# Performance work log

Hardware: AMD Instinct MI355X
Metric: run time of the kernel (lower is better)

The kernel has to match this reference:

```python
import jax, jax.numpy as jnp
import numpy as np

B, S, D, H = 2, 2048, 1024, 16
HD = D // H  # head_dim = 64
ROPE_BASE = 10000.0
INIT_STD = 0.02


def setup_inputs() -> dict:
    key = jax.random.key(0)
    k1, k2, k3 = jax.random.split(key, 3)
    x = jax.random.normal(k1, (B, S, D), dtype=jnp.float32)
    w_qkv = jax.random.normal(k2, (3 * D, D), dtype=jnp.float32) * INIT_STD
    w_out = jax.random.normal(k3, (D, D), dtype=jnp.float32) * (1.0 / np.sqrt(D))
    b_out = jnp.zeros((D,), dtype=jnp.float32)
    return {"x": x, "w_qkv": w_qkv, "w_out": w_out, "b_out": b_out}


def _rope_cos_sin(s_len, head_dim, dtype):
    theta = 1.0 / ROPE_BASE ** (jnp.arange(0, head_dim, 2, dtype=jnp.float32) / head_dim)
    freqs = jnp.outer(jnp.arange(s_len, dtype=jnp.float32), theta)  # [s, d/2]
    freqs = jnp.concatenate([freqs, freqs], axis=-1)  # [s, d]
    return jnp.cos(freqs).astype(dtype), jnp.sin(freqs).astype(dtype)


def _apply_rope(qk, cos, sin):
    # qk: [b, h, s, d]; rotate-half: (-x2, x1)
    d2 = qk.shape[-1] // 2
    x1, x2 = qk[..., :d2], qk[..., d2:]
    rot = jnp.concatenate([-x2, x1], axis=-1)
    return qk * cos + rot * sin


def reference(x, w_qkv, w_out, b_out):
    b, s, d = x.shape
    qkv = jnp.einsum('bsd,ed->bse', x, w_qkv)  # [b, s, 3D]
    qkv = qkv.reshape(b, s, 3 * H, HD).transpose(0, 2, 1, 3)  # [b, 3h, s, d]
    qk, v = qkv[:, :2 * H], qkv[:, 2 * H:]
    cos, sin = _rope_cos_sin(s, HD, x.dtype)
    qk = _apply_rope(qk, cos, sin)
    q, k = qk[:, :H], qk[:, H:]
    scale = 1.0 / np.sqrt(HD)
    scores = jnp.einsum('bhqd,bhkd->bhqk', q, k) * scale  # [b, h, s, s]
    causal = jnp.tril(jnp.ones((s, s), dtype=bool))
    scores = jnp.where(causal, scores, jnp.finfo(scores.dtype).min)
    attn = jax.nn.softmax(scores, axis=-1)
    o = jnp.einsum('bhqk,bhkd->bhqd', attn, v)  # [b, h, s, d]
    o = o.transpose(0, 2, 1, 3).reshape(b, s, d)
    return jnp.einsum('bsd,ed->bse', o, w_out) + b_out
```

## Files before the change

kernel.cpp:

```cpp
#include <hip/hip_runtime.h>
#include <hip/hip_fp16.h>
#include <math.h>

#define B_  2
#define S_  2048
#define D_  1024
#define H_  16
#define HD_ 64

typedef _Float16  f16;
typedef __attribute__((ext_vector_type(8))) _Float16 f16x8;
typedef __attribute__((ext_vector_type(4))) _Float16 f16x4;
typedef __attribute__((ext_vector_type(4))) float    f32x4;

#define LOG2E 1.4426950408889634f
#define L2_10000_DIV32 0.41524101186092029f

__device__ __forceinline__ float fin(float v) { return (v == v) ? v : 0.0f; }

__device__ __forceinline__ f16x8 cvt8(const float* p) {
  float4 a = *(const float4*)p;
  float4 b = *(const float4*)(p + 4);
  f16x8 h;
  h[0] = (f16)a.x; h[1] = (f16)a.y; h[2] = (f16)a.z; h[3] = (f16)a.w;
  h[4] = (f16)b.x; h[5] = (f16)b.y; h[6] = (f16)b.z; h[7] = (f16)b.w;
  return h;
}

__device__ __forceinline__ int swz64(int r, int c) {
  return r * 64 + ((((c >> 3) ^ (r & 7)) << 3) | (c & 7));
}

#define GLD16(g, l)                                                        \
  __builtin_amdgcn_global_load_lds(                                        \
      (const __attribute__((address_space(1))) void*)(g),                  \
      (__attribute__((address_space(3))) void*)(l), 16, 0, 0)

__global__ void __launch_bounds__(256)
k_cvt3(const float* __restrict__ wq, const float* __restrict__ wo,
       const float* __restrict__ x,
       f16* __restrict__ wqh, f16* __restrict__ woh, f16* __restrict__ xh,
       float2* __restrict__ tab, int doX)
{
  const int NWQ = 3 * D_ * D_ / 4, NWO = D_ * D_ / 4, NX = B_ * S_ * D_ / 4;
  const int n = NWQ + NWO + (doX ? NX : 0);
  for (int i = blockIdx.x * 256 + threadIdx.x; i < n; i += gridDim.x * 256) {
    const float* src; f16* dst; int j;
    if (i < NWQ)            { src = wq; dst = wqh; j = i; }
    else if (i < NWQ + NWO) { src = wo; dst = woh; j = i - NWQ; }
    else                    { src = x;  dst = xh;  j = i - NWQ - NWO; }
    float4 v = ((const float4*)src)[j];
    f16x4 h = {(f16)v.x, (f16)v.y, (f16)v.z, (f16)v.w};
    ((f16x4*)dst)[j] = h;
  }
  for (int i = blockIdx.x * 256 + threadIdx.x; i < S_ * 32; i += gridDim.x * 256) {
    const int p = i >> 5, j = i & 31;
    const float th = exp2f(-(float)j * L2_10000_DIV32);
    float s, c;
    sincosf((float)p * th, &s, &c);
    tab[i] = make_float2(c, s);
  }
}

template <bool XF16>
__global__ void __launch_bounds__(256)
k_qkv4(const float* __restrict__ xf, const f16* __restrict__ xh,
       const f16* __restrict__ wqh, const float2* __restrict__ tab,
       f16* __restrict__ Qb, f16* __restrict__ Kb, f16* __restrict__ Vt)
{
  __shared__ __align__(16) f16 As[2][128 * 64];
  __shared__ __align__(16) f16 Bs[2][128 * 64];
  const int t = threadIdx.x;
  const int w = t >> 6;
  const int lane = t & 63;
  const int ll = lane & 15;
  const int quad = lane >> 4;
  const int wm = w >> 1, wn = w & 1;
  const int row0 = blockIdx.y * 128;
  const int col0 = blockIdx.x * 128;

  const f32x4 fz = {0.f, 0.f, 0.f, 0.f};
  f32x4 acc[4][4];
#pragma unroll
  for (int i = 0; i < 4; ++i)
#pragma unroll
    for (int j = 0; j < 4; ++j) acc[i][j] = fz;

  const int rO = lane >> 3;
  const int gc = (lane & 7) ^ rO;
  const f16* pA = xh  + (size_t)(row0 + w * 8 + rO) * D_ + gc * 8;
  const f16* pB = wqh + (size_t)(col0 + w * 8 + rO) * D_ + gc * 8;
  const int ldst = (w * 8) * 64;

  const int raA0 = swz64(ll, quad * 8);
  const int raA1 = swz64(ll, 32 + quad * 8);

  const int ldr = t >> 3;
  const int ldk = (t & 7) * 8;
  const float* gaf = xf + (size_t)(row0 + ldr) * D_ + ldk;

  if (XF16) {
#pragma unroll
    for (int i = 0; i < 4; ++i) {
      GLD16(pA + (size_t)(i * 32) * D_, &As[0][i * 32 * 64 + ldst]);
      GLD16(pB + (size_t)(i * 32) * D_, &Bs[0][i * 32 * 64 + ldst]);
    }
    __syncthreads();
    pA += 64; pB += 64;

    for (int kt = 0; kt < 16; ++kt) {
      const int cur = kt & 1, nxt = cur ^ 1;
      if (kt < 15) {
#pragma unroll
        for (int i = 0; i < 4; ++i) {
          GLD16(pA + (size_t)(i * 32) * D_, &As[nxt][i * 32 * 64 + ldst]);
          GLD16(pB + (size_t)(i * 32) * D_, &Bs[nxt][i * 32 * 64 + ldst]);
        }
        pA += 64; pB += 64;
      }
      const f16* Ac = &As[cur][0];
      const f16* Bc = &Bs[cur][0];
#pragma unroll
      for (int kk = 0; kk < 2; ++kk) {
        const int ro = kk ? raA1 : raA0;
        f16x8 a[4], b[4];
#pragma unroll
        for (int mt = 0; mt < 4; ++mt)
          a[mt] = *(const f16x8*)&Ac[(wm * 64 + mt * 16) * 64 + ro];
#pragma unroll
        for (int nt = 0; nt < 4; ++nt)
          b[nt] = *(const f16x8*)&Bc[(wn * 64 + nt * 16) * 64 + ro];
#pragma unroll
        for (int mt = 0; mt < 4; ++mt)
#pragma unroll
          for (int nt = 0; nt < 4; ++nt)
            acc[mt][nt] = __builtin_amdgcn_mfma_f32_16x16x32_f16(
                a[mt], b[nt], acc[mt][nt], 0, 0, 0);
      }
      __syncthreads();
    }
  } else {
    for (int kt = 0; kt < D_; kt += 64) {
      f16x8 ra[4];
#pragma unroll
      for (int i = 0; i < 4; ++i)
        ra[i] = cvt8(gaf + (size_t)i * 32 * D_ + kt);
      __syncthreads();
#pragma unroll
      for (int i = 0; i < 4; ++i) {
        *(f16x8*)&As[0][swz64(i * 32 + ldr, ldk)] = ra[i];
        GLD16(pB + (size_t)(i * 32) * D_ + kt, &Bs[0][i * 32 * 64 + ldst]);
      }
      __syncthreads();
#pragma unroll
      for (int kk = 0; kk < 2; ++kk) {
        const int ro = kk ? raA1 : raA0;
        f16x8 a[4], b[4];
#pragma unroll
        for (int mt = 0; mt < 4; ++mt)
          a[mt] = *(const f16x8*)&As[0][(wm * 64 + mt * 16) * 64 + ro];
#pragma unroll
        for (int nt = 0; nt < 4; ++nt)
          b[nt] = *(const f16x8*)&Bs[0][(wn * 64 + nt * 16) * 64 + ro];
#pragma unroll
        for (int mt = 0; mt < 4; ++mt)
#pragma unroll
          for (int nt = 0; nt < 4; ++nt)
            acc[mt][nt] = __builtin_amdgcn_mfma_f32_16x16x32_f16(
                a[mt], b[nt], acc[mt][nt], 0, 0, 0);
      }
      __syncthreads();
    }
  }

  const int h3 = (col0 >> 6) + wn;
  if (h3 < 32) {
    f16* dst = (h3 < 16) ? Qb : Kb;
    const int h = (h3 < 16) ? h3 : h3 - 16;
#pragma unroll
    for (int mt = 0; mt < 4; ++mt) {
#pragma unroll
      for (int r = 0; r < 4; ++r) {
        const int row = row0 + wm * 64 + mt * 16 + quad * 4 + r;
        const int b = row >> 11;
        const int p = row & (S_ - 1);
        f16* base = dst + ((size_t)(b * H_ + h) * S_ + p) * HD_;
        const float2 cs0 = tab[p * 32 + ll];
        const float2 cs1 = tab[p * 32 + 16 + ll];
        {
          float x1 = acc[mt][0][r], x2 = acc[mt][2][r];
          base[ll]      = (f16)fin(x1 * cs0.x - x2 * cs0.y);
          base[ll + 32] = (f16)fin(x2 * cs0.x + x1 * cs0.y);
        }
        {
          float x1 = acc[mt][1][r], x2 = acc[mt][3][r];
          base[16 + ll]      = (f16)fin(x1 * cs1.x - x2 * cs1.y);
          base[16 + ll + 32] = (f16)fin(x2 * cs1.x + x1 * cs1.y);
        }
      }
    }
  } else {
    const int hv = h3 - 32;
#pragma unroll
    for (int mt = 0; mt < 4; ++mt)
#pragma unroll
      for (int nt = 0; nt < 4; ++nt)
#pragma unroll
        for (int r = 0; r < 4; ++r) {
          const int row = row0 + wm * 64 + mt * 16 + quad * 4 + r;
          const int b = row >> 11;
          const int p = row & (S_ - 1);
          const int dd = nt * 16 + ll;
          Vt[((size_t)(b * H_ + hv) * HD_ + dd) * S_ + p] = (f16)fin(acc[mt][nt][r]);
        }
  }
}

__device__ __forceinline__ bool softmax_tile7(
    f32x4 sc[4], bool diag, int qloc, int quad,
    float& mrun, float& lrun, float& alpha, f16* const pst[4])
{
  if (diag) {
#pragma unroll
    for (int nt = 0; nt < 4; ++nt)
#pragma unroll
      for (int r = 0; r < 4; ++r)
        if ((nt * 16 + quad * 4 + r) > qloc) sc[nt][r] = -3.0e4f;
  }
  float pm = mrun;
#pragma unroll
  for (int nt = 0; nt < 4; ++nt)
#pragma unroll
    for (int r = 0; r < 4; ++r) pm = fmaxf(pm, sc[nt][r]);
  pm = fmaxf(pm, __shfl_xor(pm, 16));
  pm = fmaxf(pm, __shfl_xor(pm, 32));
  const bool resc = !__all(pm <= mrun + 8.0f);
  if (resc) { alpha = exp2f(mrun - pm); mrun = pm; }
  float ps = 0.f;
#pragma unroll
  for (int nt = 0; nt < 4; ++nt) {
    f16x4 pk;
#pragma unroll
    for (int r = 0; r < 4; ++r) {
      float p = exp2f(sc[nt][r] - mrun);
      ps += p;
      pk[r] = (f16)p;
    }
    *(f16x4*)pst[nt] = pk;
  }
  ps += __shfl_xor(ps, 16);
  ps += __shfl_xor(ps, 32);
  lrun = (resc ? lrun * alpha : lrun) + ps;
  return resc;
}

__device__ __forceinline__ void write_o7(
    f32x4 acco[4], float lrun, f16* const pst[4],
    const f16* pb0, const f16* pb1,
    int ll, int quad, int w, int qt, size_t bh, f16* Ob)
{
  const float inv = 1.0f / fmaxf(lrun, 1e-30f);
#pragma unroll
  for (int dg = 0; dg < 4; ++dg) {
    f16x4 ov;
#pragma unroll
    for (int r = 0; r < 4; ++r) ov[r] = (f16)fin(acco[dg][r] * inv);
    *(f16x4*)pst[dg] = ov;
  }
  const size_t row = bh * S_ + qt * 64 + w * 16 + ll;
  f16x8 o0 = *(const f16x8*)pb0;
  f16x8 o1 = *(const f16x8*)pb1;
  *(f16x8*)&Ob[row * HD_ + quad * 8]      = o0;
  *(f16x8*)&Ob[row * HD_ + 32 + quad * 8] = o1;
}

#define ABODY(KB0, KB1, VB0, VB1, WKA, WKB, WVA, WVB, PRE, DIAG)           \
  do {                                                                     \
    f16x8 nk0, nk1, nv0, nv1;                                              \
    if (PRE) {                                                             \
      nk0 = *(const f16x8*)pK; nk1 = *(const f16x8*)(pK + 8);              \
    }                                                                      \
    f16x8 ak[2][4];                                                        \
    _Pragma("unroll")                                                      \
    for (int nt = 0; nt < 4; ++nt) {                                       \
      ak[0][nt] = *(const f16x8*)(KB0 + nt * 1024);                        \
      ak[1][nt] = *(const f16x8*)(KB1 + nt * 1024);                        \
    }                                                                      \
    f32x4 s[4] = {fz, fz, fz, fz};                                         \
    __builtin_amdgcn_s_setprio(1);                                         \
    _Pragma("unroll")                                                      \
    for (int k2 = 0; k2 < 2; ++k2)                                         \
      _Pragma("unroll")                                                    \
      for (int nt = 0; nt < 4; ++nt)                                       \
        s[nt] = __builtin_amdgcn_mfma_f32_16x16x32_f16(                    \
            ak[k2][nt], bq[k2], s[nt], 0, 0, 0);                           \
    __builtin_amdgcn_s_setprio(0);                                         \
    if (PRE) {                                                             \
      nv0 = *(const f16x8*)pV; nv1 = *(const f16x8*)(pV + 8);              \
      pK += 64 * HD_; pV += 64;                                            \
    }                                                                      \
    float alpha;                                                           \
    const bool resc = softmax_tile7(s, DIAG, qloc, quad, m, l, alpha, pst);\
    if (resc) {                                                            \
      _Pragma("unroll")                                                    \
      for (int dg = 0; dg < 4; ++dg)                                       \
        _Pragma("unroll")                                                  \
        for (int r = 0; r < 4; ++r) acco[dg][r] *= alpha;                  \
    }                                                                      \
    f16x8 av[2][4];                                                        \
    _Pragma("unroll")                                                      \
    for (int dg = 0; dg < 4; ++dg) {                                       \
      av[0][dg] = *(const f16x8*)(VB0 + dg * 1024);                        \
      av[1][dg] = *(const f16x8*)(VB1 + dg * 1024);                        \
    }                                                                      \
    f16x8 bp0 = *(const f16x8*)pb0;                                        \
    f16x8 bp1 = *(const f16x8*)pb1;                                        \
    __builtin_amdgcn_s_setprio(1);                                         \
    _Pragma("unroll")                                                      \
    for (int dg = 0; dg < 4; ++dg)                                         \
      acco[dg] = __builtin_amdgcn_mfma_f32_16x16x32_f16(                   \
          av[0][dg], bp0, acco[dg], 0, 0, 0);                              \
    _Pragma("unroll")                                                      \
    for (int dg = 0; dg < 4; ++dg)                                         \
      acco[dg] = __builtin_amdgcn_mfma_f32_16x16x32_f16(                   \
          av[1][dg], bp1, acco[dg], 0, 0, 0);                              \
    __builtin_amdgcn_s_setprio(0);                                         \
    if (PRE) {                                                             \
      *(f16x8*)WKA = nk0; *(f16x8*)WKB = nk1;                              \
      *(f16x8*)WVA = nv0; *(f16x8*)WVB = nv1;                              \
    }                                                                      \
    __syncthreads();                                                       \
  } while (0)

#define ABODY_B0(PRE, DIAG) \
  ABODY(kb00, kb01, vb00, vb01, wk1a, wk1b, wv1a, wv1b, PRE, DIAG)
#define ABODY_B1(PRE, DIAG) \
  ABODY(kb10, kb11, vb10, vb11, wk0a, wk0b, wv0a, wv0b, PRE, DIAG)

__global__ void __launch_bounds__(256, 4)
k_attn7(const f16* Qb, const f16* __restrict__ Kb,
        const f16* __restrict__ Vt, f16* Ob)
{
  __shared__ __align__(16) f16 Ks[2][64 * 64];
  __shared__ __align__(16) f16 Vs[2][64 * 64];
  __shared__ __align__(16) f16 Ps[4][16 * 64];

  const int t = threadIdx.x;
  const int w = t >> 6;
  const int lane = t & 63;
  const int ll = lane & 15;
  const int quad = lane >> 4;
  const int bx = blockIdx.x;
  const int base = (bx & 1) ? 31 - (bx >> 1) : (bx >> 1);
  const int qt = ((int)blockIdx.y < 8) ? base : 31 - base;
  const int h = blockIdx.y;
  const int b = blockIdx.z;
  const size_t bh = (size_t)b * H_ + h;
  const f16* Qg = Qb + bh * S_ * HD_;
  const f16* Kg = Kb + bh * S_ * HD_;
  const f16* Vg = Vt + bh * HD_ * S_;

  f16x8 bq[2];
  {
    const f16 hsc = (f16)(0.125f * LOG2E);
#pragma unroll
    for (int k2 = 0; k2 < 2; ++k2) {
      bq[k2] = *(const f16x8*)(Qg + (size_t)(qt * 64 + w * 16 + ll) * HD_ + k2 * 32 + quad * 8);
#pragma unroll
      for (int e = 0; e < 8; ++e) bq[k2][e] *= hsc;
    }
  }

  f16* Pt = &Ps[w][0];
  const f16* kb00 = &Ks[0][swz64(ll, quad * 8)];
  const f16* kb01 = &Ks[0][swz64(ll, 32 + quad * 8)];
  const f16* kb10 = &Ks[1][swz64(ll, quad * 8)];
  const f16* kb11 = &Ks[1][swz64(ll, 32 + quad * 8)];
  const f16* vb00 = &Vs[0][swz64(ll, quad * 8)];
  const f16* vb01 = &Vs[0][swz64(ll, 32 + quad * 8)];
  const f16* vb10 = &Vs[1][swz64(ll, quad * 8)];
  const f16* vb11 = &Vs[1][swz64(ll, 32 + quad * 8)];
  const f16* pb0  = &Pt[swz64(ll, quad * 8)];
  const f16* pb1  = &Pt[swz64(ll, 32 + quad * 8)];
  f16* pst[4] = { &Pt[swz64(ll, 0 * 16 + quad * 4)],
                  &Pt[swz64(ll, 1 * 16 + quad * 4)],
                  &Pt[swz64(ll, 2 * 16 + quad * 4)],
                  &Pt[swz64(ll, 3 * 16 + quad * 4)] };
  const int sr = t >> 2;
  const int scc = (t & 3) * 16;
  f16* wk0a = &Ks[0][swz64(sr, scc)];
  f16* wk0b = &Ks[0][swz64(sr, scc + 8)];
  f16* wk1a = &Ks[1][swz64(sr, scc)];
  f16* wk1b = &Ks[1][swz64(sr, scc + 8)];
  f16* wv0a = &Vs[0][swz64(sr, scc)];
  f16* wv0b = &Vs[0][swz64(sr, scc + 8)];
  f16* wv1a = &Vs[1][swz64(sr, scc)];
  f16* wv1b = &Vs[1][swz64(sr, scc + 8)];

  {
    f16x8 a0 = *(const f16x8*)(Kg + (size_t)sr * HD_ + scc);
    f16x8 a1 = *(const f16x8*)(Kg + (size_t)sr * HD_ + scc + 8);
    f16x8 b0 = *(const f16x8*)(Vg + (size_t)sr * S_ + scc);
    f16x8 b1 = *(const f16x8*)(Vg + (size_t)sr * S_ + scc + 8);
    *(f16x8*)wk0a = a0;
    *(f16x8*)wk0b = a1;
    *(f16x8*)wv0a = b0;
    *(f16x8*)wv0b = b1;
  }
  __syncthreads();

  const f16* pK = Kg + (size_t)(64 + sr) * HD_ + scc;
  const f16* pV = Vg + (size_t)sr * S_ + 64 + scc;

  const f32x4 fz = {0.f, 0.f, 0.f, 0.f};
  f32x4 acco[4] = {fz, fz, fz, fz};
  float m = -3.0e4f, l = 0.f;
  const int qloc = w * 16 + ll;

  int j = 0;
  while (j + 1 < qt) {
    ABODY_B0(true, false);
    ABODY_B1(true, false);
    j += 2;
  }
  if (j < qt) {
    ABODY_B0(true, false);
    ++j;
    ABODY_B1(false, true);
  } else {
    ABODY_B0(false, true);
  }

  write_o7(acco, l, pst, pb0, pb1, ll, quad, w, qt, bh, Ob);
}

__global__ void __launch_bounds__(256)
k_out4(const f16* __restrict__ Ob, const f16* __restrict__ Wh,
       const float* __restrict__ bias, float* __restrict__ out)
{
  __shared__ __align__(16) f16 As[2][64 * 64];
  __shared__ __align__(16) f16 Bs[2][128 * 64];
  const int t = threadIdx.x;
  const int w = t >> 6;
  const int lane = t & 63;
  const int ll = lane & 15;
  const int quad = lane >> 4;
  const int wm = w >> 1, wn = w & 1;
  const int row0 = blockIdx.y * 64;
  const int col0 = blockIdx.x * 128;
  const int bb = row0 >> 11;
  const int s0 = row0 & (S_ - 1);

  const f32x4 fz = {0.f, 0.f, 0.f, 0.f};
  f32x4 acc[2][4];
#pragma unroll
  for (int i = 0; i < 2; ++i)
#pragma unroll
    for (int j = 0; j < 4; ++j) acc[i][j] = fz;

  const int rO = lane >> 3;
  const int gc = (lane & 7) ^ rO;
  const int ldst = (w * 8) * 64;
  const f16* pB = Wh + (size_t)(col0 + w * 8 + rO) * D_ + gc * 8;
  const f16* pA = Ob + (((size_t)(bb * H_)) * S_ + s0 + w * 8 + rO) * HD_ + gc * 8;

  const int raA0 = swz64(ll, quad * 8);
  const int raA1 = swz64(ll, 32 + quad * 8);

#pragma unroll
  for (int i = 0; i < 2; ++i)
    GLD16(pA + (size_t)(i * 32) * HD_, &As[0][i * 32 * 64 + ldst]);
#pragma unroll
  for (int i = 0; i < 4; ++i)
    GLD16(pB + (size_t)(i * 32) * D_, &Bs[0][i * 32 * 64 + ldst]);
  __syncthreads();
  pA += (size_t)S_ * HD_;
  pB += 64;

  for (int kt = 0; kt < 16; ++kt) {
    const int cur = kt & 1, nxt = cur ^ 1;
    if (kt < 15) {
#pragma unroll
      for (int i = 0; i < 2; ++i)
        GLD16(pA + (size_t)(i * 32) * HD_, &As[nxt][i * 32 * 64 + ldst]);
#pragma unroll
      for (int i = 0; i < 4; ++i)
        GLD16(pB + (size_t)(i * 32) * D_, &Bs[nxt][i * 32 * 64 + ldst]);
      pA += (size_t)S_ * HD_;
      pB += 64;
    }
    const f16* Ac = &As[cur][0];
    const f16* Bc = &Bs[cur][0];
#pragma unroll
    for (int kk = 0; kk < 2; ++kk) {
      const int ro = kk ? raA1 : raA0;
      f16x8 a[2], b[4];
#pragma unroll
      for (int mt = 0; mt < 2; ++mt)
        a[mt] = *(const f16x8*)&Ac[(wm * 32 + mt * 16) * 64 + ro];
#pragma unroll
      for (int nt = 0; nt < 4; ++nt)
        b[nt] = *(const f16x8*)&Bc[(wn * 64 + nt * 16) * 64 + ro];
#pragma unroll
      for (int mt = 0; mt < 2; ++mt)
#pragma unroll
        for (int nt = 0; nt < 4; ++nt)
          acc[mt][nt] = __builtin_amdgcn_mfma_f32_16x16x32_f16(
              a[mt], b[nt], acc[mt][nt], 0, 0, 0);
    }
    __syncthreads();
  }

#pragma unroll
  for (int mt = 0; mt < 2; ++mt)
#pragma unroll
    for (int r = 0; r < 4; ++r) {
      const int row = row0 + wm * 32 + mt * 16 + quad * 4 + r;
#pragma unroll
      for (int nt = 0; nt < 4; ++nt) {
        const int col = col0 + wn * 64 + nt * 16 + ll;
        out[(size_t)row * D_ + col] = fin(acc[mt][nt][r] + bias[col]);
      }
    }
}

extern "C" void kernel_launch(void* const* d_in, const int* in_sizes, int n_in,
                              void* d_out, int out_size, void* d_ws, size_t ws_size,
                              hipStream_t stream) {
  const float* x    = (const float*)d_in[0];
  const float* wqkv = (const float*)d_in[1];
  const float* wout = (const float*)d_in[2];
  const float* bout = (const float*)d_in[3];
  float* out = (float*)d_out;

  char* ws = (char*)d_ws;
  f16* wqh = (f16*)(ws);
  f16* Qb  = (f16*)(ws + 6291456);
  f16* Kb  = (f16*)(ws + 14680064);
  f16* Vt  = (f16*)(ws + 23068672);
  f16* woh = (f16*)(ws + 31457280);
  const bool bigws = ws_size >= (size_t)41943040;
  f16* xh  = (f16*)(ws + 33554432);

  float2* tab = (float2*)((char*)d_out + 9437184);

  k_cvt3<<<2048, 256, 0, stream>>>(wqkv, wout, x, wqh, woh, xh, tab, bigws ? 1 : 0);
  if (bigws)
    k_qkv4<true><<<dim3(3 * D_ / 128, (B_ * S_) / 128), 256, 0, stream>>>(
        x, xh, wqh, tab, Qb, Kb, Vt);
  else
    k_qkv4<false><<<dim3(3 * D_ / 128, (B_ * S_) / 128), 256, 0, stream>>>(
        x, xh, wqh, tab, Qb, Kb, Vt);
  k_attn7<<<dim3(32, H_, B_), 256, 0, stream>>>(Qb, Kb, Vt, Qb );
  k_out4<<<dim3(D_ / 128, (B_ * S_) / 64), 256, 0, stream>>>(
      Qb, woh, bout, out);
}
```

Measured before the change: 201.9 us.

## Remap GEMM block order per XCD, fine-grain waits in QKV, single-buffer out-proj

The QKV GEMM block IDs are remapped so consecutive tiles land on the same XCD, which should improve L2 reuse. Its __syncthreads are replaced with explicit vmcnt/lgkmcnt waits plus raw barriers, so the prefetch of the next tile stays in flight while the current one is computed. The output projection drops double buffering for a single-buffered load/sync/compute loop and also gets the XCD-aware block remap. That lowers LDS use, possibly raising occupancy, but it gives up load/compute overlap in that kernel.

```diff
diff --git a/kernel.cpp b/kernel.cpp
--- a/kernel.cpp
+++ b/kernel.cpp
@@ -35,6 +35,9 @@
   __builtin_amdgcn_global_load_lds(                                        \
       (const __attribute__((address_space(1))) void*)(g),                  \
       (__attribute__((address_space(3))) void*)(l), 16, 0, 0)
+
+#define VMWAIT(N) asm volatile("s_waitcnt vmcnt(" #N ")" ::: "memory")
+#define LGKM0()   asm volatile("s_waitcnt lgkmcnt(0)" ::: "memory")
 
 __global__ void __launch_bounds__(256)
 k_cvt3(const float* __restrict__ wq, const float* __restrict__ wo,
@@ -64,7 +67,7 @@
 
 template <bool XF16>
 __global__ void __launch_bounds__(256)
-k_qkv4(const float* __restrict__ xf, const f16* __restrict__ xh,
+k_qkv5(const float* __restrict__ xf, const f16* __restrict__ xh,
        const f16* __restrict__ wqh, const float2* __restrict__ tab,
        f16* __restrict__ Qb, f16* __restrict__ Kb, f16* __restrict__ Vt)
 {
@@ -76,8 +79,11 @@
   const int ll = lane & 15;
   const int quad = lane >> 4;
   const int wm = w >> 1, wn = w & 1;
-  const int row0 = blockIdx.y * 128;
-  const int col0 = blockIdx.x * 128;
+
+  const int flat  = blockIdx.y * 24 + blockIdx.x;
+  const int newid = (flat & 7) * 96 + (flat >> 3);
+  const int row0 = (newid / 24) * 128;
+  const int col0 = (newid % 24) * 128;
 
   const f32x4 fz = {0.f, 0.f, 0.f, 0.f};
   f32x4 acc[4][4];
@@ -105,7 +111,8 @@
       GLD16(pA + (size_t)(i * 32) * D_, &As[0][i * 32 * 64 + ldst]);
       GLD16(pB + (size_t)(i * 32) * D_, &Bs[0][i * 32 * 64 + ldst]);
     }
-    __syncthreads();
+    VMWAIT(0);
+    __builtin_amdgcn_s_barrier();
     pA += 64; pB += 64;
 
     for (int kt = 0; kt < 16; ++kt) {
@@ -117,7 +124,12 @@
           GLD16(pB + (size_t)(i * 32) * D_, &Bs[nxt][i * 32 * 64 + ldst]);
         }
         pA += 64; pB += 64;
+        VMWAIT(8);
+      } else {
+        VMWAIT(0);
       }
+      __builtin_amdgcn_s_barrier();
+
       const f16* Ac = &As[cur][0];
       const f16* Bc = &Bs[cur][0];
 #pragma unroll
@@ -137,7 +149,8 @@
             acc[mt][nt] = __builtin_amdgcn_mfma_f32_16x16x32_f16(
                 a[mt], b[nt], acc[mt][nt], 0, 0, 0);
       }
-      __syncthreads();
+      LGKM0();
+      __builtin_amdgcn_s_barrier();
     }
   } else {
     for (int kt = 0; kt < D_; kt += 64) {
@@ -435,19 +448,22 @@
 }
 
 __global__ void __launch_bounds__(256)
-k_out4(const f16* __restrict__ Ob, const f16* __restrict__ Wh,
+k_out3(const f16* __restrict__ Ob, const f16* __restrict__ Wh,
        const float* __restrict__ bias, float* __restrict__ out)
 {
-  __shared__ __align__(16) f16 As[2][64 * 64];
-  __shared__ __align__(16) f16 Bs[2][128 * 64];
+  __shared__ __align__(16) f16 As[64 * 64];
+  __shared__ __align__(16) f16 Bs[128 * 64];
   const int t = threadIdx.x;
   const int w = t >> 6;
   const int lane = t & 63;
   const int ll = lane & 15;
   const int quad = lane >> 4;
   const int wm = w >> 1, wn = w & 1;
-  const int row0 = blockIdx.y * 64;
-  const int col0 = blockIdx.x * 128;
+
+  const int flat  = blockIdx.y * 8 + blockIdx.x;
+  const int newid = (flat & 7) * 64 + (flat >> 3);
+  const int row0 = (newid >> 3) * 64;
+  const int col0 = (newid & 7) * 128;
   const int bb = row0 >> 11;
   const int s0 = row0 & (S_ - 1);
 
@@ -460,47 +476,27 @@
 
   const int rO = lane >> 3;
   const int gc = (lane & 7) ^ rO;
-  const int ldst = (w * 8) * 64;
-  const f16* pB = Wh + (size_t)(col0 + w * 8 + rO) * D_ + gc * 8;
-  const f16* pA = Ob + (((size_t)(bb * H_)) * S_ + s0 + w * 8 + rO) * HD_ + gc * 8;
-
-  const int raA0 = swz64(ll, quad * 8);
-  const int raA1 = swz64(ll, 32 + quad * 8);
-
-#pragma unroll
-  for (int i = 0; i < 2; ++i)
-    GLD16(pA + (size_t)(i * 32) * HD_, &As[0][i * 32 * 64 + ldst]);
-#pragma unroll
-  for (int i = 0; i < 4; ++i)
-    GLD16(pB + (size_t)(i * 32) * D_, &Bs[0][i * 32 * 64 + ldst]);
-  __syncthreads();
-  pA += (size_t)S_ * HD_;
-  pB += 64;
+  const f16* gb2 = Wh + (size_t)(col0 + w * 8 + rO) * D_ + gc * 8;
 
   for (int kt = 0; kt < 16; ++kt) {
-    const int cur = kt & 1, nxt = cur ^ 1;
-    if (kt < 15) {
-#pragma unroll
-      for (int i = 0; i < 2; ++i)
-        GLD16(pA + (size_t)(i * 32) * HD_, &As[nxt][i * 32 * 64 + ldst]);
-#pragma unroll
-      for (int i = 0; i < 4; ++i)
-        GLD16(pB + (size_t)(i * 32) * D_, &Bs[nxt][i * 32 * 64 + ldst]);
-      pA += (size_t)S_ * HD_;
-      pB += 64;
-    }
-    const f16* Ac = &As[cur][0];
-    const f16* Bc = &Bs[cur][0];
-#pragma unroll
-    for (int kk = 0; kk < 2; ++kk) {
-      const int ro = kk ? raA1 : raA0;
+    const f16* ga2 = Ob + (((size_t)(bb * H_ + kt)) * S_ + s0 + w * 8 + rO) * HD_ + gc * 8;
+    __syncthreads();
+#pragma unroll
+    for (int i = 0; i < 2; ++i)
+      GLD16(ga2 + (size_t)(i * 32) * HD_, &As[(i * 32 + w * 8) * 64]);
+#pragma unroll
+    for (int i = 0; i < 4; ++i)
+      GLD16(gb2 + (size_t)(i * 32) * D_ + kt * 64, &Bs[(i * 32 + w * 8) * 64]);
+    __syncthreads();
+#pragma unroll
+    for (int kk = 0; kk < 64; kk += 32) {
       f16x8 a[2], b[4];
 #pragma unroll
       for (int mt = 0; mt < 2; ++mt)
-        a[mt] = *(const f16x8*)&Ac[(wm * 32 + mt * 16) * 64 + ro];
+        a[mt] = *(const f16x8*)&As[swz64(wm * 32 + mt * 16 + ll, kk + quad * 8)];
 #pragma unroll
       for (int nt = 0; nt < 4; ++nt)
-        b[nt] = *(const f16x8*)&Bc[(wn * 64 + nt * 16) * 64 + ro];
+        b[nt] = *(const f16x8*)&Bs[swz64(wn * 64 + nt * 16 + ll, kk + quad * 8)];
 #pragma unroll
       for (int mt = 0; mt < 2; ++mt)
 #pragma unroll
@@ -508,7 +504,6 @@
           acc[mt][nt] = __builtin_amdgcn_mfma_f32_16x16x32_f16(
               a[mt], b[nt], acc[mt][nt], 0, 0, 0);
     }
-    __syncthreads();
   }
 
 #pragma unroll
@@ -546,12 +541,12 @@
 
   k_cvt3<<<2048, 256, 0, stream>>>(wqkv, wout, x, wqh, woh, xh, tab, bigws ? 1 : 0);
   if (bigws)
-    k_qkv4<true><<<dim3(3 * D_ / 128, (B_ * S_) / 128), 256, 0, stream>>>(
+    k_qkv5<true><<<dim3(3 * D_ / 128, (B_ * S_) / 128), 256, 0, stream>>>(
         x, xh, wqh, tab, Qb, Kb, Vt);
   else
-    k_qkv4<false><<<dim3(3 * D_ / 128, (B_ * S_) / 128), 256, 0, stream>>>(
+    k_qkv5<false><<<dim3(3 * D_ / 128, (B_ * S_) / 128), 256, 0, stream>>>(
         x, xh, wqh, tab, Qb, Kb, Vt);
   k_attn7<<<dim3(32, H_, B_), 256, 0, stream>>>(Qb, Kb, Vt, Qb );
-  k_out4<<<dim3(D_ / 128, (B_ * S_) / 64), 256, 0, stream>>>(
+  k_out3<<<dim3(D_ / 128, (B_ * S_) / 64), 256, 0, stream>>>(
       Qb, woh, bout, out);
 }
```

Result: faster. 184.6 us (-8.6%).
